# Optimization experiments

Measured on AMD Instinct MI355X. Metric: run time of the kernel, lower is better.

Reference implementation:

```python
import jax, jax.numpy as jnp
import numpy as np

B, C, H, W = 32, 512, 64, 64
P = 8            # partition (window) size
HEAD_DIM = 32
N_HEADS = C // HEAD_DIM  # 16
MLP_RATIO = 4
LN_EPS = 1e-5


def _rel_pos_index(p):
    # Swin/MaxViT-style relative position index for a p x p window -> [p*p, p*p]
    coords = np.stack(np.meshgrid(np.arange(p), np.arange(p), indexing='ij'), 0).reshape(2, -1)
    rel = coords[:, :, None] - coords[:, None, :]          # [2, pp, pp]
    rel = rel.transpose(1, 2, 0) + (p - 1)                 # shift to >= 0
    idx = rel[..., 0] * (2 * p - 1) + rel[..., 1]          # [pp, pp]
    return jnp.asarray(idx, jnp.int32)


def setup_inputs() -> dict:
    key = jax.random.key(0)
    ks = jax.random.split(key, 10)
    s = 0.02
    d_ff = MLP_RATIO * C
    inp = {
        'x': jax.random.normal(ks[0], (B, C, H, W), jnp.float32),
        'gamma1': jnp.ones((C,), jnp.float32),
        'beta1': jnp.zeros((C,), jnp.float32),
        'gamma2': jnp.ones((C,), jnp.float32),
        'beta2': jnp.zeros((C,), jnp.float32),
        'qkv_w': jax.random.normal(ks[1], (C, 3 * C), jnp.float32) * s,
        'qkv_b': jnp.zeros((3 * C,), jnp.float32),
        'merge_w': jax.random.normal(ks[2], (C, C), jnp.float32) * s,
        'merge_b': jnp.zeros((C,), jnp.float32),
        'bias_table': jax.random.normal(ks[3], ((2 * P - 1) ** 2, N_HEADS), jnp.float32) * s,
        'w1': jax.random.normal(ks[4], (C, d_ff), jnp.float32) * s,
        'b1': jnp.zeros((d_ff,), jnp.float32),
        'w2': jax.random.normal(ks[5], (d_ff, C), jnp.float32) * s,
        'b2': jnp.zeros((C,), jnp.float32),
        'rel_idx': _rel_pos_index(P),
    }
    return inp


def _layernorm(t, g, b):
    mu = jnp.mean(t, axis=-1, keepdims=True)
    var = jnp.mean(jnp.square(t - mu), axis=-1, keepdims=True)
    return (t - mu) * jax.lax.rsqrt(var + LN_EPS) * g + b


def reference(x, gamma1, beta1, gamma2, beta2, qkv_w, qkv_b, merge_w, merge_b,
              bias_table, w1, b1, w2, b2, rel_idx):
    p, hd, nh = P, HEAD_DIM, N_HEADS
    Bx, Cx, Hx, Wx = x.shape
    hp, wp = Hx // p, Wx // p
    G, PP = hp * wp, p * p

    # --- window partition: [B,C,H,W] -> [B, G, p*p, C] (partition_type='window', no swap)
    xw = x.reshape(Bx, Cx, hp, p, wp, p).transpose(0, 2, 4, 3, 5, 1).reshape(Bx, G, PP, Cx)

    # --- relative-position multi-head attention on norm1(x)
    h = _layernorm(xw, gamma1, beta1)
    qkv = h @ qkv_w + qkv_b                                   # [B,G,PP,3C]
    q, k, v = jnp.split(qkv, 3, axis=-1)
    q = q.reshape(Bx, G, PP, nh, hd) * (hd ** -0.5)
    k = k.reshape(Bx, G, PP, nh, hd)
    v = v.reshape(Bx, G, PP, nh, hd)
    attn = jnp.einsum('bgqhd,bgkhd->bghqk', q, k)             # [B,G,nh,PP,PP]
    bias = bias_table[rel_idx]                                # [PP,PP,nh]
    attn = attn + bias.transpose(2, 0, 1)[None, None]
    attn = jax.nn.softmax(attn, axis=-1)
    o = jnp.einsum('bghqk,bgkhd->bgqhd', attn, v).reshape(Bx, G, PP, Cx)
    xw = xw + (o @ merge_w + merge_b)                          # residual (dropout/SD p=0)

    # --- MLP block on norm2(x)
    h2 = _layernorm(xw, gamma2, beta2)
    m = jax.nn.gelu(h2 @ w1 + b1) @ w2 + b2
    xw = xw + m

    # --- window departition: [B,G,p*p,C] -> [B,C,H,W]
    out = xw.reshape(Bx, hp, wp, p, p, Cx).transpose(0, 5, 1, 3, 2, 4).reshape(Bx, Cx, Hx, Wx)
    return out
```

## Files before the change

kernel.cpp:

```cpp
#include <hip/hip_runtime.h>
#include <stdint.h>

typedef __attribute__((ext_vector_type(8))) short short8;
typedef __attribute__((ext_vector_type(4))) float f32x4;
typedef __attribute__((address_space(3))) void lds_void;
typedef __attribute__((address_space(1))) void gv_void;

static __device__ __forceinline__ float bf2f(unsigned short u) {
    union { uint32_t i; float f; } v; v.i = ((uint32_t)u) << 16; return v.f;
}
static __device__ __forceinline__ unsigned short f2bf(float f) {
    union { float f; uint32_t i; } v; v.f = f;
    uint32_t i = v.i;
    uint32_t r = (i + 0x7fffu + ((i >> 16) & 1u)) >> 16;
    return (unsigned short)r;
}
static __device__ __forceinline__ float fexp(float x) {
    float r;
    asm("v_exp_f32 %0, %1" : "=v"(r) : "v"(x * 1.44269504088896f));
    return r;
}
static __device__ __forceinline__ float frcp(float x) {
    float r;
    asm("v_rcp_f32 %0, %1" : "=v"(r) : "v"(x));
    return r;
}

__global__ void k_detect(const void* __restrict__ g1, int* __restrict__ flag) {
    if (threadIdx.x == 0 && blockIdx.x == 0) {
        const unsigned short* u = (const unsigned short*)g1;
        flag[0] = (u[0] == 0x3F80u) ? 0 : 1;
    }
}

__global__ __launch_bounds__(256) void k_cvt(const void* __restrict__ src,
                                             unsigned short* __restrict__ dst,
                                             int n, const int* __restrict__ flag) {
    int i = blockIdx.x * 256 + threadIdx.x;
    if (i < n) {
        dst[i] = flag[0] ? f2bf(((const float*)src)[i])
                         : ((const unsigned short*)src)[i];
    }
}

__global__ __launch_bounds__(256) void k_transpose(const void* __restrict__ in,
                                                   unsigned short* __restrict__ out,
                                                   int R, int C, const int* __restrict__ flag) {
    __shared__ unsigned short tile[32][33];
    int isf = flag[0];
    int tx = threadIdx.x, ty = threadIdx.y;
    int x = blockIdx.x * 32 + tx;
    int y0 = blockIdx.y * 32;
    for (int j = ty; j < 32; j += 8) {
        size_t idx = (size_t)(y0 + j) * C + x;
        tile[j][tx] = isf ? f2bf(((const float*)in)[idx]) : ((const unsigned short*)in)[idx];
    }
    __syncthreads();
    int x2 = y0 + tx;
    int y20 = blockIdx.x * 32;
    for (int j = ty; j < 32; j += 8)
        out[(size_t)(y20 + j) * R + x2] = tile[tx][j];
}

__global__ __launch_bounds__(256) void k_prep_bias(const void* __restrict__ bias_table,
                                                   const int* __restrict__ rel_idx,
                                                   float* __restrict__ biasp,
                                                   const int* __restrict__ flag) {
    int i = blockIdx.x * 256 + threadIdx.x;
    int isf = flag[0];
    int h = i & 15, qk = i >> 4;
    size_t idx = (size_t)rel_idx[qk] * 16 + h;
    float v = isf ? ((const float*)bias_table)[idx] : bf2f(((const unsigned short*)bias_table)[idx]);
    biasp[h * 4096 + qk] = v;
}

__global__ __launch_bounds__(256) void k_partition_ln(const void* __restrict__ x,
                                                      const unsigned short* __restrict__ g1,
                                                      const unsigned short* __restrict__ b1,
                                                      unsigned short* __restrict__ xw,
                                                      unsigned short* __restrict__ h,
                                                      int b0, const int* __restrict__ flag) {
    __shared__ unsigned short tile[64][512];
    int isf = flag[0];
    int bh = blockIdx.x, bl = bh >> 6, hh = bh & 63;
    int b = b0 + bl;
    int tid = threadIdx.x;
    size_t xoff = (((size_t)b * 512) * 64 + hh) * 64;
    int c0 = tid >> 3, ch = tid & 7;
    if (isf) {
        const float* xb = (const float*)x + xoff;
        for (int k = 0; k < 16; ++k) {
            int c = c0 + k * 32;
            f32x4 v0 = *reinterpret_cast<const f32x4*>(xb + (size_t)c * 4096 + ch * 8);
            f32x4 v1 = *reinterpret_cast<const f32x4*>(xb + (size_t)c * 4096 + ch * 8 + 4);
#pragma unroll
            for (int j = 0; j < 4; ++j) tile[ch * 8 + j][c] = f2bf(v0[j]);
#pragma unroll
            for (int j = 0; j < 4; ++j) tile[ch * 8 + 4 + j][c] = f2bf(v1[j]);
        }
    } else {
        const unsigned short* xb = (const unsigned short*)x + xoff;
        for (int k = 0; k < 16; ++k) {
            int c = c0 + k * 32;
            short8 v = *reinterpret_cast<const short8*>(xb + (size_t)c * 4096 + ch * 8);
#pragma unroll
            for (int j = 0; j < 8; ++j) tile[ch * 8 + j][c] = (unsigned short)v[j];
        }
    }
    __syncthreads();
    int w = tid >> 2, q = tid & 3;
    float s = 0.f, s2 = 0.f;
#pragma unroll 4
    for (int j = 0; j < 128; ++j) {
        int c = q * 128 + ((j + 8 * w) & 127);
        float f = bf2f(tile[w][c]);
        s += f; s2 += f * f;
    }
    s += __shfl_xor(s, 1);  s += __shfl_xor(s, 2);
    s2 += __shfl_xor(s2, 1); s2 += __shfl_xor(s2, 2);
    float mu = s * (1.f / 512.f);
    float rstd = rsqrtf(s2 * (1.f / 512.f) - mu * mu + 1e-5f);
    int t = (bl * 64 + (hh >> 3) * 8 + (w >> 3)) * 64 + (hh & 7) * 8 + (w & 7);
    unsigned short* xr = xw + (size_t)t * 512;
    unsigned short* hr = h + (size_t)t * 512;
    for (int cc = q * 128; cc < q * 128 + 128; cc += 8) {
        short8 raw, hn;
#pragma unroll
        for (int j = 0; j < 8; ++j) {
            unsigned short u = tile[w][cc + j];
            raw[j] = (short)u;
            float f = (bf2f(u) - mu) * rstd * bf2f(g1[cc + j]) + bf2f(b1[cc + j]);
            hn[j] = (short)f2bf(f);
        }
        *reinterpret_cast<short8*>(xr + cc) = raw;
        *reinterpret_cast<short8*>(hr + cc) = hn;
    }
}

__global__ __launch_bounds__(256) void k_ln(const unsigned short* __restrict__ in,
                                            const unsigned short* __restrict__ g,
                                            const unsigned short* __restrict__ b,
                                            unsigned short* __restrict__ out) {
    int wid = threadIdx.x >> 6, lane = threadIdx.x & 63;
    size_t t = (size_t)blockIdx.x * 4 + wid;
    short8 v = *reinterpret_cast<const short8*>(in + t * 512 + lane * 8);
    float f[8], s = 0.f, s2 = 0.f;
#pragma unroll
    for (int j = 0; j < 8; ++j) { f[j] = bf2f((unsigned short)v[j]); s += f[j]; s2 += f[j] * f[j]; }
    for (int m = 1; m < 64; m <<= 1) { s += __shfl_xor(s, m); s2 += __shfl_xor(s2, m); }
    float mu = s * (1.f / 512.f);
    float rstd = rsqrtf(s2 * (1.f / 512.f) - mu * mu + 1e-5f);
    short8 ov;
#pragma unroll
    for (int j = 0; j < 8; ++j)
        ov[j] = (short)f2bf((f[j] - mu) * rstd * bf2f(g[lane * 8 + j]) + bf2f(b[lane * 8 + j]));
    *reinterpret_cast<short8*>(out + t * 512 + lane * 8) = ov;
}

template <int MODE>
__global__ __launch_bounds__(512, 2) void k_gemm4(const unsigned short* __restrict__ A,
                                                  const unsigned short* __restrict__ BT,
                                                  const unsigned short* __restrict__ bias,
                                                  const unsigned short* __restrict__ res,
                                                  unsigned short* __restrict__ out,
                                                  int M, int N, int K) {
    __shared__ unsigned short AsS[2][16384];
    __shared__ unsigned short BsS[2][16384];
    const int tid = threadIdx.x, lane = tid & 63, wid = tid >> 6;

    int nwg = gridDim.x * gridDim.y;
    int lin = blockIdx.y * gridDim.x + blockIdx.x;
    int swz = (lin & 7) * (nwg >> 3) + (lin >> 3);
    int mt = swz % gridDim.x, nt = swz / gridDim.x;

    const int wr = wid >> 2, wc = wid & 3;
    const int rl = lane & 15, qg = lane >> 4;

    const int srow = tid >> 3;
    const int scb  = (tid & 7) ^ (srow & 7);
    const unsigned short* Agb = A  + ((size_t)mt * 256 + srow) * K + scb * 8;
    const unsigned short* Bgb = BT + ((size_t)nt * 256 + srow) * K + scb * 8;

    f32x4 acc[8][4];
#pragma unroll
    for (int mf = 0; mf < 8; ++mf)
#pragma unroll
        for (int nf = 0; nf < 4; ++nf) {
            acc[mf][nf][0] = 0.f; acc[mf][nf][1] = 0.f; acc[mf][nf][2] = 0.f; acc[mf][nf][3] = 0.f;
        }

    const int NT = K >> 6;

    auto stage = [&](int t, int buf) {
#pragma unroll
        for (int s = 0; s < 4; ++s) {
            __builtin_amdgcn_global_load_lds((const gv_void*)(Agb + (size_t)s * 64 * K + t * 64),
                                             (lds_void*)(&AsS[buf][s * 4096 + tid * 8]), 16, 0, 0);
            __builtin_amdgcn_global_load_lds((const gv_void*)(Bgb + (size_t)s * 64 * K + t * 64),
                                             (lds_void*)(&BsS[buf][s * 4096 + tid * 8]), 16, 0, 0);
        }
    };

    stage(0, 0);
    asm volatile("s_waitcnt vmcnt(0)" ::: "memory");
    __builtin_amdgcn_s_barrier();
    asm volatile("" ::: "memory");

    const int arow0 = wr * 128 + rl;
    const int brow0 = wc * 64 + rl;
    const int rx = rl & 7;

    for (int t = 0; t < NT; ++t) {
        int cur = t & 1;
        if (t + 1 < NT) stage(t + 1, cur ^ 1);
#pragma unroll
        for (int ks = 0; ks < 2; ++ks) {
            const int kb = ((ks * 4 + qg) ^ rx) * 8;
            short8 af[8], bfr[4];
#pragma unroll
            for (int mf = 0; mf < 8; ++mf)
                af[mf] = *reinterpret_cast<const short8*>(&AsS[cur][(arow0 + mf * 16) * 64 + kb]);
#pragma unroll
            for (int nf = 0; nf < 4; ++nf)
                bfr[nf] = *reinterpret_cast<const short8*>(&BsS[cur][(brow0 + nf * 16) * 64 + kb]);
            __builtin_amdgcn_s_setprio(1);
#pragma unroll
            for (int mf = 0; mf < 8; ++mf)
#pragma unroll
                for (int nf = 0; nf < 4; ++nf)
                    acc[mf][nf] = __builtin_amdgcn_mfma_f32_16x16x32_bf16(af[mf], bfr[nf], acc[mf][nf], 0, 0, 0);
            __builtin_amdgcn_s_setprio(0);
        }
        asm volatile("s_waitcnt vmcnt(0)" ::: "memory");
        __builtin_amdgcn_s_barrier();
        asm volatile("" ::: "memory");
    }

    const int PST = 264;
    unsigned short* pb = (unsigned short*)AsS;
    float bz[4];
#pragma unroll
    for (int nf = 0; nf < 4; ++nf) bz[nf] = bf2f(bias[nt * 256 + wc * 64 + nf * 16 + rl]);
    int row_l = tid >> 4, cbl = (tid & 15) * 16;
    int growb = mt * 256 + (row_l >> 4) * 128 + (row_l & 15);
    size_t gcol = (size_t)nt * 256 + cbl;

#pragma unroll
    for (int mf = 0; mf < 8; ++mf) {
        __syncthreads();
#pragma unroll
        for (int nf = 0; nf < 4; ++nf)
#pragma unroll
            for (int r = 0; r < 4; ++r) {
                float v = acc[mf][nf][r] + bz[nf];
                if (MODE == 2) {
                    float z = 0.7978845608f * (v + 0.044715f * v * v * v);
                    float e = fexp(-2.0f * z);
                    v = v * frcp(1.f + e);
                }
                pb[(wr * 16 + qg * 4 + r) * PST + wc * 64 + nf * 16 + rl] = f2bf(v);
            }
        __syncthreads();
        size_t go = (size_t)(growb + mf * 16) * N + gcol;
        short8 o1 = *reinterpret_cast<const short8*>(&pb[row_l * PST + cbl]);
        short8 o2 = *reinterpret_cast<const short8*>(&pb[row_l * PST + cbl + 8]);
        if (MODE == 1) {
            short8 r1 = *reinterpret_cast<const short8*>(&res[go]);
            short8 r2 = *reinterpret_cast<const short8*>(&res[go + 8]);
#pragma unroll
            for (int j = 0; j < 8; ++j) {
                o1[j] = (short)f2bf(bf2f((unsigned short)o1[j]) + bf2f((unsigned short)r1[j]));
                o2[j] = (short)f2bf(bf2f((unsigned short)o2[j]) + bf2f((unsigned short)r2[j]));
            }
        }
        *reinterpret_cast<short8*>(&out[go]) = o1;
        *reinterpret_cast<short8*>(&out[go + 8]) = o2;
    }
}

__global__ __launch_bounds__(64) void k_attn(const unsigned short* __restrict__ qkv,
                                             const float* __restrict__ biasp,
                                             unsigned short* __restrict__ o) {
    __shared__ unsigned short Pl[64][72];
    int blk = blockIdx.x;
    int head = blk & 15, win = blk >> 4;
    size_t T0 = (size_t)win * 64;
    int lane = threadIdx.x;
    int rl = lane & 15, qg = lane >> 4;
    const unsigned short* base = qkv + T0 * 1536;
    int qoff = head * 32, koff = 512 + head * 32, voff = 1024 + head * 32;

    f32x4 s[4][4];
#pragma unroll
    for (int m = 0; m < 4; ++m)
#pragma unroll
        for (int n = 0; n < 4; ++n) { s[m][n][0] = 0.f; s[m][n][1] = 0.f; s[m][n][2] = 0.f; s[m][n][3] = 0.f; }

    short8 aq[4], bk[4];
#pragma unroll
    for (int m = 0; m < 4; ++m)
        aq[m] = *reinterpret_cast<const short8*>(base + (size_t)(16 * m + rl) * 1536 + qoff + qg * 8);
#pragma unroll
    for (int n = 0; n < 4; ++n)
        bk[n] = *reinterpret_cast<const short8*>(base + (size_t)(16 * n + rl) * 1536 + koff + qg * 8);
#pragma unroll
    for (int m = 0; m < 4; ++m)
#pragma unroll
        for (int n = 0; n < 4; ++n)
            s[m][n] = __builtin_amdgcn_mfma_f32_16x16x32_bf16(aq[m], bk[n], s[m][n], 0, 0, 0);

    const float scale = 0.17677669529663687f;
    const float* bh = biasp + head * 4096;
#pragma unroll
    for (int m = 0; m < 4; ++m) {
#pragma unroll
        for (int r = 0; r < 4; ++r) {
            int row = 16 * m + qg * 4 + r;
            float v0 = s[m][0][r] * scale + bh[row * 64 + rl];
            float v1 = s[m][1][r] * scale + bh[row * 64 + 16 + rl];
            float v2 = s[m][2][r] * scale + bh[row * 64 + 32 + rl];
            float v3 = s[m][3][r] * scale + bh[row * 64 + 48 + rl];
            float mx = fmaxf(fmaxf(v0, v1), fmaxf(v2, v3));
            mx = fmaxf(mx, __shfl_xor(mx, 1));
            mx = fmaxf(mx, __shfl_xor(mx, 2));
            mx = fmaxf(mx, __shfl_xor(mx, 4));
            mx = fmaxf(mx, __shfl_xor(mx, 8));
            v0 = fexp(v0 - mx); v1 = fexp(v1 - mx); v2 = fexp(v2 - mx); v3 = fexp(v3 - mx);
            float sm = v0 + v1 + v2 + v3;
            sm += __shfl_xor(sm, 1);
            sm += __shfl_xor(sm, 2);
            sm += __shfl_xor(sm, 4);
            sm += __shfl_xor(sm, 8);
            float inv = frcp(sm);
            Pl[row][rl]      = f2bf(v0 * inv);
            Pl[row][16 + rl] = f2bf(v1 * inv);
            Pl[row][32 + rl] = f2bf(v2 * inv);
            Pl[row][48 + rl] = f2bf(v3 * inv);
        }
    }
    __syncthreads();

    short8 bv[2][2];
#pragma unroll
    for (int ks = 0; ks < 2; ++ks)
#pragma unroll
        for (int n2 = 0; n2 < 2; ++n2) {
            short8 t;
#pragma unroll
            for (int i = 0; i < 8; ++i)
                t[i] = (short)base[(size_t)(32 * ks + qg * 8 + i) * 1536 + voff + n2 * 16 + rl];
            bv[ks][n2] = t;
        }

    f32x4 acc2[4][2];
#pragma unroll
    for (int m = 0; m < 4; ++m)
#pragma unroll
        for (int n2 = 0; n2 < 2; ++n2) { acc2[m][n2][0] = 0.f; acc2[m][n2][1] = 0.f; acc2[m][n2][2] = 0.f; acc2[m][n2][3] = 0.f; }

#pragma unroll
    for (int m = 0; m < 4; ++m) {
        short8 p0 = *reinterpret_cast<const short8*>(&Pl[16 * m + rl][qg * 8]);
        short8 p1 = *reinterpret_cast<const short8*>(&Pl[16 * m + rl][32 + qg * 8]);
#pragma unroll
        for (int n2 = 0; n2 < 2; ++n2) {
            acc2[m][n2] = __builtin_amdgcn_mfma_f32_16x16x32_bf16(p0, bv[0][n2], acc2[m][n2], 0, 0, 0);
            acc2[m][n2] = __builtin_amdgcn_mfma_f32_16x16x32_bf16(p1, bv[1][n2], acc2[m][n2], 0, 0, 0);
        }
    }
#pragma unroll
    for (int m = 0; m < 4; ++m)
#pragma unroll
        for (int n2 = 0; n2 < 2; ++n2)
#pragma unroll
            for (int r = 0; r < 4; ++r) {
                int row = 16 * m + qg * 4 + r;
                o[(T0 + row) * 512 + head * 32 + n2 * 16 + rl] = f2bf(acc2[m][n2][r]);
            }
}

__global__ __launch_bounds__(256) void k_departition(const unsigned short* __restrict__ tok,
                                                     void* __restrict__ xo,
                                                     int b0, const int* __restrict__ flag) {
    __shared__ unsigned short tile[64][512];
    int isf = flag[0];
    int bh = blockIdx.x, bl = bh >> 6, hh = bh & 63;
    int b = b0 + bl;
    int tid = threadIdx.x;
    int Tb = (bl * 64 + (hh >> 3) * 8) * 64 + (hh & 7) * 8;
    for (int k = 0; k < 16; ++k) {
        int flat = k * 256 + tid;
        int w = flat >> 6, ch = flat & 63;
        int t = Tb + (w >> 3) * 64 + (w & 7);
        short8 v = *reinterpret_cast<const short8*>(tok + (size_t)t * 512 + ch * 8);
        *reinterpret_cast<short8*>(&tile[w][ch * 8]) = v;
    }
    __syncthreads();
    size_t xoff = (((size_t)b * 512) * 64 + hh) * 64;
    if (isf) {
        float* xb = (float*)xo + xoff;
        for (int k = 0; k < 16; ++k) {
            int flat = k * 256 + tid;
            int c = flat >> 3, wc = flat & 7;
            f32x4 a, d;
#pragma unroll
            for (int j = 0; j < 4; ++j) a[j] = bf2f(tile[wc * 8 + j][c]);
#pragma unroll
            for (int j = 0; j < 4; ++j) d[j] = bf2f(tile[wc * 8 + 4 + j][c]);
            *reinterpret_cast<f32x4*>(xb + (size_t)c * 4096 + wc * 8) = a;
            *reinterpret_cast<f32x4*>(xb + (size_t)c * 4096 + wc * 8 + 4) = d;
        }
    } else {
        unsigned short* xb = (unsigned short*)xo + xoff;
        for (int k = 0; k < 16; ++k) {
            int flat = k * 256 + tid;
            int c = flat >> 3, wc = flat & 7;
            short8 v;
#pragma unroll
            for (int j = 0; j < 8; ++j) v[j] = (short)tile[wc * 8 + j][c];
            *reinterpret_cast<short8*>(xb + (size_t)c * 4096 + wc * 8) = v;
        }
    }
}

extern "C" void kernel_launch(void* const* d_in, const int* in_sizes, int n_in,
                              void* d_out, int out_size, void* d_ws, size_t ws_size,
                              hipStream_t stream) {
    const void* x          = d_in[0];
    const void* g1         = d_in[1];
    const void* be1        = d_in[2];
    const void* g2         = d_in[3];
    const void* be2        = d_in[4];
    const void* qkv_w      = d_in[5];
    const void* qkv_b      = d_in[6];
    const void* merge_w    = d_in[7];
    const void* merge_b    = d_in[8];
    const void* bias_table = d_in[9];
    const void* w1         = d_in[10];
    const void* b1         = d_in[11];
    const void* w2         = d_in[12];
    const void* b2         = d_in[13];
    const int*  rel_idx    = (const int*)d_in[14];

    const size_t extra = 8u << 20;
    int CB = 4;
    if      (ws_size >= (size_t)131072 * 10240 + extra) CB = 32;
    else if (ws_size >= (size_t)65536  * 10240 + extra) CB = 16;
    else if (ws_size >= (size_t)32768  * 10240 + extra) CB = 8;
    int nch = 32 / CB;
    size_t tok = (size_t)CB * 4096;

    unsigned short* xw_c     = (unsigned short*)d_ws;
    unsigned short* h_c      = xw_c + tok * 512;
    unsigned short* o_c      = h_c + tok * 512;
    unsigned short* qkv_c    = o_c + tok * 512;
    unsigned short* mid_c    = qkv_c + tok * 1536;
    unsigned short* qkv_wT   = mid_c + tok * 2048;
    unsigned short* merge_wT = qkv_wT + 1536 * 512;
    unsigned short* w1T      = merge_wT + 512 * 512;
    unsigned short* w2T      = w1T + 2048 * 512;
    unsigned short* vecs     = w2T + 512 * 2048;
    float*          biasp    = (float*)(vecs + 6656);
    int*            flag     = (int*)(biasp + 65536);

    unsigned short* ng1 = vecs + 0,    *nbe1 = vecs + 512;
    unsigned short* ng2 = vecs + 1024, *nbe2 = vecs + 1536;
    unsigned short* nqb = vecs + 2048, *nmb  = vecs + 3584;
    unsigned short* nb1 = vecs + 4096, *nb2  = vecs + 6144;

    k_detect<<<1, 64, 0, stream>>>(g1, flag);
    k_cvt<<<2, 256, 0, stream>>>(g1, ng1, 512, flag);
    k_cvt<<<2, 256, 0, stream>>>(be1, nbe1, 512, flag);
    k_cvt<<<2, 256, 0, stream>>>(g2, ng2, 512, flag);
    k_cvt<<<2, 256, 0, stream>>>(be2, nbe2, 512, flag);
    k_cvt<<<6, 256, 0, stream>>>(qkv_b, nqb, 1536, flag);
    k_cvt<<<2, 256, 0, stream>>>(merge_b, nmb, 512, flag);
    k_cvt<<<8, 256, 0, stream>>>(b1, nb1, 2048, flag);
    k_cvt<<<2, 256, 0, stream>>>(b2, nb2, 512, flag);
    k_transpose<<<dim3(48, 16), dim3(32, 8), 0, stream>>>(qkv_w, qkv_wT, 512, 1536, flag);
    k_transpose<<<dim3(16, 16), dim3(32, 8), 0, stream>>>(merge_w, merge_wT, 512, 512, flag);
    k_transpose<<<dim3(64, 16), dim3(32, 8), 0, stream>>>(w1, w1T, 512, 2048, flag);
    k_transpose<<<dim3(16, 64), dim3(32, 8), 0, stream>>>(w2, w2T, 2048, 512, flag);
    k_prep_bias<<<256, 256, 0, stream>>>(bias_table, rel_idx, biasp, flag);

    int mtiles = (int)(tok / 256);
    int M = (int)tok;
    for (int c = 0; c < nch; ++c) {
        int b0 = c * CB;
        k_partition_ln<<<CB * 64, 256, 0, stream>>>(x, ng1, nbe1, xw_c, h_c, b0, flag);
        k_gemm4<0><<<dim3(mtiles, 6), 512, 0, stream>>>(h_c, qkv_wT, nqb, nullptr, qkv_c, M, 1536, 512);
        k_attn<<<CB * 1024, 64, 0, stream>>>(qkv_c, biasp, o_c);
        k_gemm4<1><<<dim3(mtiles, 2), 512, 0, stream>>>(o_c, merge_wT, nmb, xw_c, xw_c, M, 512, 512);
        k_ln<<<(int)(tok / 4), 256, 0, stream>>>(xw_c, ng2, nbe2, h_c);
        k_gemm4<2><<<dim3(mtiles, 8), 512, 0, stream>>>(h_c, w1T, nb1, nullptr, mid_c, M, 2048, 512);
        k_gemm4<1><<<dim3(mtiles, 2), 512, 0, stream>>>(mid_c, w2T, nb2, xw_c, qkv_c, M, 512, 2048);
        k_departition<<<CB * 64, 256, 0, stream>>>(qkv_c, d_out, b0, flag);
    }
}
```

Measured before the change: 1.937 ms.

## Restructure GEMM main loop into 4-stage K=32 LDS pipeline and cap chunk size

The GEMM kernel switches from a double-buffered K=64 tile to a four-deep ring of K=32 slices in one 128 KB LDS array. It keeps three slices in flight and uses graded vmcnt waits so global loads overlap more compute, with a new XOR swizzle for the 32-wide rows. Launch bounds drop to one block per CU because of the larger LDS footprint. The host also limits the batch chunk size to at most 8 images, which cuts working-set size but adds more launches per forward pass.

```diff
diff --git a/kernel.cpp b/kernel.cpp
--- a/kernel.cpp
+++ b/kernel.cpp
@@ -158,14 +158,13 @@
 }
 
 template <int MODE>
-__global__ __launch_bounds__(512, 2) void k_gemm4(const unsigned short* __restrict__ A,
+__global__ __launch_bounds__(512, 1) void k_gemm5(const unsigned short* __restrict__ A,
                                                   const unsigned short* __restrict__ BT,
                                                   const unsigned short* __restrict__ bias,
                                                   const unsigned short* __restrict__ res,
                                                   unsigned short* __restrict__ out,
                                                   int M, int N, int K) {
-    __shared__ unsigned short AsS[2][16384];
-    __shared__ unsigned short BsS[2][16384];
+    __shared__ unsigned short S[65536];
     const int tid = threadIdx.x, lane = tid & 63, wid = tid >> 6;
 
     int nwg = gridDim.x * gridDim.y;
@@ -176,10 +175,11 @@
     const int wr = wid >> 2, wc = wid & 3;
     const int rl = lane & 15, qg = lane >> 4;
 
-    const int srow = tid >> 3;
-    const int scb  = (tid & 7) ^ (srow & 7);
-    const unsigned short* Agb = A  + ((size_t)mt * 256 + srow) * K + scb * 8;
-    const unsigned short* Bgb = BT + ((size_t)nt * 256 + srow) * K + scb * 8;
+    const int strow = tid >> 2;
+    const int scb   = (tid & 3) ^ ((tid >> 3) & 3);
+    const unsigned short* Agb = A  + ((size_t)mt * 256 + strow) * K + scb * 8;
+    const unsigned short* Bgb = BT + ((size_t)nt * 256 + strow) * K + scb * 8;
+    const int ldst = strow * 32 + (tid & 3) * 8;
 
     f32x4 acc[8][4];
 #pragma unroll
@@ -189,55 +189,63 @@
             acc[mf][nf][0] = 0.f; acc[mf][nf][1] = 0.f; acc[mf][nf][2] = 0.f; acc[mf][nf][3] = 0.f;
         }
 
-    const int NT = K >> 6;
-
-    auto stage = [&](int t, int buf) {
-#pragma unroll
-        for (int s = 0; s < 4; ++s) {
-            __builtin_amdgcn_global_load_lds((const gv_void*)(Agb + (size_t)s * 64 * K + t * 64),
-                                             (lds_void*)(&AsS[buf][s * 4096 + tid * 8]), 16, 0, 0);
-            __builtin_amdgcn_global_load_lds((const gv_void*)(Bgb + (size_t)s * 64 * K + t * 64),
-                                             (lds_void*)(&BsS[buf][s * 4096 + tid * 8]), 16, 0, 0);
+    const int NH = K >> 5;
+
+    auto stage = [&](int h) {
+        int base = (h & 3) * 16384;
+#pragma unroll
+        for (int s = 0; s < 2; ++s) {
+            __builtin_amdgcn_global_load_lds((const gv_void*)(Agb + (size_t)s * 128 * K + h * 32),
+                                             (lds_void*)(&S[base + s * 4096 + ldst]), 16, 0, 0);
+            __builtin_amdgcn_global_load_lds((const gv_void*)(Bgb + (size_t)s * 128 * K + h * 32),
+                                             (lds_void*)(&S[base + 8192 + s * 4096 + ldst]), 16, 0, 0);
         }
     };
 
-    stage(0, 0);
-    asm volatile("s_waitcnt vmcnt(0)" ::: "memory");
-    __builtin_amdgcn_s_barrier();
-    asm volatile("" ::: "memory");
+    stage(0); stage(1); stage(2);
 
     const int arow0 = wr * 128 + rl;
     const int brow0 = wc * 64 + rl;
-    const int rx = rl & 7;
-
-    for (int t = 0; t < NT; ++t) {
-        int cur = t & 1;
-        if (t + 1 < NT) stage(t + 1, cur ^ 1);
-#pragma unroll
-        for (int ks = 0; ks < 2; ++ks) {
-            const int kb = ((ks * 4 + qg) ^ rx) * 8;
-            short8 af[8], bfr[4];
-#pragma unroll
-            for (int mf = 0; mf < 8; ++mf)
-                af[mf] = *reinterpret_cast<const short8*>(&AsS[cur][(arow0 + mf * 16) * 64 + kb]);
-#pragma unroll
-            for (int nf = 0; nf < 4; ++nf)
-                bfr[nf] = *reinterpret_cast<const short8*>(&BsS[cur][(brow0 + nf * 16) * 64 + kb]);
-            __builtin_amdgcn_s_setprio(1);
-#pragma unroll
-            for (int mf = 0; mf < 8; ++mf)
-#pragma unroll
-                for (int nf = 0; nf < 4; ++nf)
-                    acc[mf][nf] = __builtin_amdgcn_mfma_f32_16x16x32_bf16(af[mf], bfr[nf], acc[mf][nf], 0, 0, 0);
-            __builtin_amdgcn_s_setprio(0);
-        }
-        asm volatile("s_waitcnt vmcnt(0)" ::: "memory");
+    const int kbr = (qg ^ ((rl >> 1) & 3)) * 8;
+
+    for (int h = 0; h < NH; ++h) {
+        const unsigned short* sA = &S[(h & 3) * 16384];
+        const unsigned short* sB = sA + 8192;
+        if (h + 3 < NH) {
+            stage(h + 3);
+            asm volatile("s_waitcnt vmcnt(12)" ::: "memory");
+        } else if (h + 2 < NH) {
+            asm volatile("s_waitcnt vmcnt(8)" ::: "memory");
+        } else if (h + 1 < NH) {
+            asm volatile("s_waitcnt vmcnt(4)" ::: "memory");
+        } else {
+            asm volatile("s_waitcnt vmcnt(0)" ::: "memory");
+        }
         __builtin_amdgcn_s_barrier();
         asm volatile("" ::: "memory");
+
+        short8 af[8], bfr[4];
+#pragma unroll
+        for (int nf = 0; nf < 4; ++nf)
+            bfr[nf] = *reinterpret_cast<const short8*>(&sB[(brow0 + nf * 16) * 32 + kbr]);
+#pragma unroll
+        for (int mf = 0; mf < 8; ++mf)
+            af[mf] = *reinterpret_cast<const short8*>(&sA[(arow0 + mf * 16) * 32 + kbr]);
+
+        __builtin_amdgcn_s_setprio(1);
+#pragma unroll
+        for (int mf = 0; mf < 8; ++mf)
+#pragma unroll
+            for (int nf = 0; nf < 4; ++nf)
+                acc[mf][nf] = __builtin_amdgcn_mfma_f32_16x16x32_bf16(af[mf], bfr[nf], acc[mf][nf], 0, 0, 0);
+        __builtin_amdgcn_s_setprio(0);
+
+        __builtin_amdgcn_s_barrier();
+        asm volatile("" ::: "memory");
     }
 
     const int PST = 264;
-    unsigned short* pb = (unsigned short*)AsS;
+    unsigned short* pb = (unsigned short*)S;
     float bz[4];
 #pragma unroll
     for (int nf = 0; nf < 4; ++nf) bz[nf] = bf2f(bias[nt * 256 + wc * 64 + nf * 16 + rl]);
@@ -444,9 +452,7 @@
 
     const size_t extra = 8u << 20;
     int CB = 4;
-    if      (ws_size >= (size_t)131072 * 10240 + extra) CB = 32;
-    else if (ws_size >= (size_t)65536  * 10240 + extra) CB = 16;
-    else if (ws_size >= (size_t)32768  * 10240 + extra) CB = 8;
+    if (ws_size >= (size_t)32768 * 10240 + extra) CB = 8;
     int nch = 32 / CB;
     size_t tok = (size_t)CB * 4096;
 
@@ -488,12 +494,12 @@
     for (int c = 0; c < nch; ++c) {
         int b0 = c * CB;
         k_partition_ln<<<CB * 64, 256, 0, stream>>>(x, ng1, nbe1, xw_c, h_c, b0, flag);
-        k_gemm4<0><<<dim3(mtiles, 6), 512, 0, stream>>>(h_c, qkv_wT, nqb, nullptr, qkv_c, M, 1536, 512);
+        k_gemm5<0><<<dim3(mtiles, 6), 512, 0, stream>>>(h_c, qkv_wT, nqb, nullptr, qkv_c, M, 1536, 512);
         k_attn<<<CB * 1024, 64, 0, stream>>>(qkv_c, biasp, o_c);
-        k_gemm4<1><<<dim3(mtiles, 2), 512, 0, stream>>>(o_c, merge_wT, nmb, xw_c, xw_c, M, 512, 512);
+        k_gemm5<1><<<dim3(mtiles, 2), 512, 0, stream>>>(o_c, merge_wT, nmb, xw_c, xw_c, M, 512, 512);
         k_ln<<<(int)(tok / 4), 256, 0, stream>>>(xw_c, ng2, nbe2, h_c);
-        k_gemm4<2><<<dim3(mtiles, 8), 512, 0, stream>>>(h_c, w1T, nb1, nullptr, mid_c, M, 2048, 512);
-        k_gemm4<1><<<dim3(mtiles, 2), 512, 0, stream>>>(mid_c, w2T, nb2, xw_c, qkv_c, M, 512, 2048);
+        k_gemm5<2><<<dim3(mtiles, 8), 512, 0, stream>>>(h_c, w1T, nb1, nullptr, mid_c, M, 2048, 512);
+        k_gemm5<1><<<dim3(mtiles, 2), 512, 0, stream>>>(mid_c, w2T, nb2, xw_c, qkv_c, M, 512, 2048);
         k_departition<<<CB * 64, 256, 0, stream>>>(qkv_c, d_out, b0, flag);
     }
 }
```

Result: faster. 1.870 ms (-3.4%).
